# Kernel optimization log

Measured on AMD Instinct MI355X. Metric: run time of the kernel, lower is better.

Reference implementation:

```python
import jax, jax.numpy as jnp
import numpy as np

DIM = 128
N = 4096


def setup_inputs() -> dict:
    key = jax.random.key(0)
    ks = jax.random.split(key, 12)
    d = DIM
    s = 0.02
    inp = jax.random.normal(ks[0], (N, 2 * d), dtype=jnp.float32)
    # H = myLinear: (2d -> 5d -> 1), tanh after each layer
    Hw1 = jax.random.normal(ks[1], (2 * d, 5 * d), dtype=jnp.float32) * s
    Hb1 = jax.random.normal(ks[2], (5 * d,), dtype=jnp.float32) * s
    Hw2 = jax.random.normal(ks[3], (5 * d, 1), dtype=jnp.float32) * s
    Hb2 = jax.random.normal(ks[4], (1,), dtype=jnp.float32) * s
    # augment_f: (d -> 4d -> 8d -> d*d), tanh after each layer
    Aw1 = jax.random.normal(ks[5], (d, 4 * d), dtype=jnp.float32) * s
    Ab1 = jax.random.normal(ks[6], (4 * d,), dtype=jnp.float32) * s
    Aw2 = jax.random.normal(ks[7], (4 * d, 8 * d), dtype=jnp.float32) * s
    Ab2 = jax.random.normal(ks[8], (8 * d,), dtype=jnp.float32) * s
    Aw3 = jax.random.normal(ks[9], (8 * d, d * d), dtype=jnp.float32) * s
    Ab3 = jax.random.normal(ks[10], (d * d,), dtype=jnp.float32) * s
    u = jax.random.uniform(ks[11], (d,), dtype=jnp.float32, minval=-0.001, maxval=0.001)
    return {"t": 0, "inp": inp, "Hw1": Hw1, "Hb1": Hb1, "Hw2": Hw2, "Hb2": Hb2,
            "Aw1": Aw1, "Ab1": Ab1, "Aw2": Aw2, "Ab2": Ab2, "Aw3": Aw3, "Ab3": Ab3, "u": u}


def reference(t, inp, Hw1, Hb1, Hw2, Hb2, Aw1, Ab1, Aw2, Ab2, Aw3, Ab3, u):
    d = DIM
    n = inp.shape[0]

    def H_scalar(z):  # z: [2d] -> scalar
        h = jnp.tanh(z @ Hw1 + Hb1)
        return jnp.tanh(h @ Hw2 + Hb2)[0]

    # per-sample gradient of scalar H w.r.t. input (== batch_jacobian squeeze)
    g = jax.vmap(jax.grad(H_scalar))(inp)  # [N, 2d]
    dx = g[:, :d]
    dv = -g[:, d:]

    x = inp[:, :d]
    h1 = jnp.tanh(x @ Aw1 + Ab1)            # [N, 4d]
    h2 = jnp.tanh(h1 @ Aw2 + Ab2)           # [N, 8d]
    gq = jnp.tanh(h2 @ Aw3 + Ab3).reshape(n, d, d)  # [N, d, d]
    dv = dv + jnp.einsum("nij,j->ni", gq, u)
    return jnp.concatenate([dx, dv], axis=-1)  # [N, 2d]
```

## Files before the change

kernel.cpp:

```cpp
#include <hip/hip_runtime.h>
#include <hip/hip_bf16.h>
#include <cstdint>


typedef __bf16 bf16_t;
typedef __bf16 bf16x4_t __attribute__((ext_vector_type(4)));
typedef __bf16 bf16x8_t __attribute__((ext_vector_type(8)));
typedef float f32x4_t __attribute__((ext_vector_type(4)));
typedef float f32x16_t __attribute__((ext_vector_type(16)));
typedef int intx4_t __attribute__((ext_vector_type(4)));
typedef int intx8_t __attribute__((ext_vector_type(8)));

#define DIMD 128
#define NROW 4096
#define SMEM_G64 24576
#define SMEM3_BYTES 98304

__device__ __forceinline__ float fast_tanh(float x) {
  float t = __builtin_amdgcn_exp2f(x * 2.8853900817779268f);
  return 1.f - 2.f * __builtin_amdgcn_rcpf(t + 1.f);
}

__device__ __forceinline__ uint8_t to_fp8(float x) {
  return (uint8_t)(__builtin_amdgcn_cvt_pk_fp8_f32(x, x, 0, false) & 0xff);
}

__device__ __forceinline__ uint32_t pk4_fp8(float a, float b, float c,
                                            float d) {
  uint32_t lo = (uint32_t)__builtin_amdgcn_cvt_pk_fp8_f32(a, b, 0, false);
  return (uint32_t)__builtin_amdgcn_cvt_pk_fp8_f32(c, d, lo, true);
}

__device__ __forceinline__ void g2l16(const void* gp, void* lp) {
  __builtin_amdgcn_global_load_lds(
      reinterpret_cast<__attribute__((address_space(1))) void*>(
          reinterpret_cast<uintptr_t>(gp)),
      reinterpret_cast<__attribute__((address_space(3))) void*>(
          reinterpret_cast<uintptr_t>(lp)),
      16, 0, 0);
}

template <int CTRL>
__device__ __forceinline__ float dpp_addf(float v) {
  return v + __int_as_float(__builtin_amdgcn_update_dpp(
                 0, __float_as_int(v), CTRL, 0xf, 0xf, true));
}
__device__ __forceinline__ float dpp_sum32(float v) {
  v = dpp_addf<0x111>(v);
  v = dpp_addf<0x112>(v);
  v = dpp_addf<0x114>(v);
  v = dpp_addf<0x118>(v);
  v = dpp_addf<0x142>(v);
  return v;
}

template <int EPI>
__device__ __forceinline__ void gemm64_body(char* smem, int bx, int by,
                                            const bf16_t* A, int lda,
                                            const bf16_t* B, int ldb, int K,
                                            const float* bias, void* outp,
                                            int ldo) {
  constexpr int BK = 32;
  bf16_t* As = (bf16_t*)smem;
  bf16_t* Bs = As + 3 * 2048;
  const int NT = K / BK;

  const int m0 = bx * 64;
  const int n0 = by * 64;
  const int tid = threadIdx.x;
  const int wave = tid >> 6;
  const int lane = tid & 63;
  const int wm = wave >> 1;
  const int wn = wave & 1;

  const int sr = lane >> 2;
  const int sk = (((lane & 3) ^ ((sr >> 1) & 3)) * 8);
  const int fr = lane & 15;
  const int fk = (((lane >> 4) ^ ((fr >> 1) & 3)) * 8);
  const int rb = wave * 16;

  const bf16_t* Ag = A + (size_t)(m0 + rb + sr) * lda + sk;
  const bf16_t* Bg = B + (size_t)(n0 + rb + sr) * ldb + sk;

#define G64_STAGE(buf, k0)                              \
  do {                                                  \
    g2l16(Ag + (k0), As + (buf) * 2048 + rb * BK);      \
    g2l16(Bg + (k0), Bs + (buf) * 2048 + rb * BK);      \
  } while (0)

  f32x4_t acc[2][2] = {};

  G64_STAGE(0, 0);
  G64_STAGE(1, BK);
  asm volatile("s_waitcnt vmcnt(2)" ::: "memory");
  __builtin_amdgcn_s_barrier();
  asm volatile("" ::: "memory");

  for (int t = 0; t < NT; ++t) {
    if (t + 2 < NT) G64_STAGE((t + 2) % 3, (t + 2) * BK);
    const bf16_t* Ab = As + (t % 3) * 2048;
    const bf16_t* Bb = Bs + (t % 3) * 2048;

    bf16x8_t af[2], bb[2];
#pragma unroll
    for (int u = 0; u < 2; ++u) {
      af[u] = *(const bf16x8_t*)(Ab + (wm * 32 + u * 16 + fr) * BK + fk);
      bb[u] = *(const bf16x8_t*)(Bb + (wn * 32 + u * 16 + fr) * BK + fk);
    }
#pragma unroll
    for (int i = 0; i < 2; ++i)
#pragma unroll
      for (int j = 0; j < 2; ++j)
        acc[i][j] = __builtin_amdgcn_mfma_f32_16x16x32_bf16(af[i], bb[j],
                                                            acc[i][j], 0, 0, 0);
    if (t < NT - 1) {
      if (t + 2 < NT)
        asm volatile("s_waitcnt vmcnt(2)" ::: "memory");
      else
        asm volatile("s_waitcnt vmcnt(0)" ::: "memory");
      __builtin_amdgcn_s_barrier();
      asm volatile("" ::: "memory");
    }
  }
#undef G64_STAGE

#pragma unroll
  for (int i = 0; i < 2; ++i) {
    const int row = m0 + wm * 32 + i * 16 + (lane >> 4) * 4;
#pragma unroll
    for (int j = 0; j < 2; ++j) {
      const int col = n0 + wn * 32 + j * 16 + fr;
      if constexpr (EPI == 0) {
        bf16_t* O = (bf16_t*)outp;
        const float b = bias[col];
#pragma unroll
        for (int r = 0; r < 4; ++r)
          O[(size_t)(row + r) * ldo + col] = (bf16_t)fast_tanh(acc[i][j][r] + b);
      } else {
        uint8_t* O = (uint8_t*)outp;
        const float b = bias[col];
#pragma unroll
        for (int r = 0; r < 4; ++r)
          O[(size_t)(row + r) * ldo + col] =
              to_fp8(64.f * fast_tanh(acc[i][j][r] + b));
      }
    }
  }
}

__device__ __forceinline__ void hbwd64_body(char* smem, int bx, int by,
                                            const bf16_t* A, int lda,
                                            const bf16_t* B, int ldb, int K,
                                            float* out, int ldo) {
  constexpr int BK = 32;
  bf16_t* As = (bf16_t*)smem;
  bf16_t* Bs = As + 3 * 2048;
  const int NT = K / BK;

  const int m0 = bx * 64;
  const int n0 = by * 64;
  const int tid = threadIdx.x;
  const int wave = tid >> 6;
  const int lane = tid & 63;
  const int wm = wave >> 2;
  const int wn = wave & 3;

  const int sr = lane >> 2;
  const int sk = (((lane & 3) ^ ((sr >> 1) & 3)) * 8);
  const int fr = lane & 15;
  const int fk = (((lane >> 4) ^ ((fr >> 1) & 3)) * 8);

  const int rbs = (wave & 3) * 16;
  const bf16_t* Sg = (wave < 4) ? A + (size_t)(m0 + rbs + sr) * lda + sk
                                : B + (size_t)(n0 + rbs + sr) * ldb + sk;
  bf16_t* Sl = ((wave < 4) ? As : Bs) + rbs * BK;

  f32x4_t acc[2] = {};

  g2l16(Sg, Sl);
  g2l16(Sg + BK, Sl + 2048);
  asm volatile("s_waitcnt vmcnt(1)" ::: "memory");
  __builtin_amdgcn_s_barrier();
  asm volatile("" ::: "memory");

  for (int t = 0; t < NT; ++t) {
    if (t + 2 < NT) g2l16(Sg + (t + 2) * BK, Sl + ((t + 2) % 3) * 2048);
    const bf16_t* Ab = As + (t % 3) * 2048;
    const bf16_t* Bb = Bs + (t % 3) * 2048;

    const bf16x8_t bb = *(const bf16x8_t*)(Bb + (wn * 16 + fr) * BK + fk);
#pragma unroll
    for (int u = 0; u < 2; ++u) {
      const bf16x8_t af =
          *(const bf16x8_t*)(Ab + (wm * 32 + u * 16 + fr) * BK + fk);
      acc[u] = __builtin_amdgcn_mfma_f32_16x16x32_bf16(af, bb, acc[u], 0, 0, 0);
    }
    if (t < NT - 1) {
      if (t + 2 < NT)
        asm volatile("s_waitcnt vmcnt(1)" ::: "memory");
      else
        asm volatile("s_waitcnt vmcnt(0)" ::: "memory");
      __builtin_amdgcn_s_barrier();
      asm volatile("" ::: "memory");
    }
  }

  const bool dx = (n0 < DIMD);
  const int col = n0 + wn * 16 + fr;
#pragma unroll
  for (int t = 0; t < 2; ++t) {
    const int row = m0 + wm * 32 + t * 16 + (lane >> 4) * 4;
#pragma unroll
    for (int r = 0; r < 4; ++r) {
      const size_t idx = (size_t)(row + r) * ldo + col;
      if (dx) out[idx] = acc[t][r];
      else atomicAdd(&out[idx], -acc[t][r]);
    }
  }
}

__device__ __forceinline__ void a3_body(char* smem, int bx, int by,
                                        const uint8_t* A, const uint8_t* B,
                                        float* out, const float* ab3,
                                        const float* uvec) {
  constexpr int BK = 64, K = 1024, NT = K / BK;
  uint8_t* As = (uint8_t*)smem;
  uint8_t* Bs = As + 49152;

  const int m0 = bx * 256;
  const int n0 = by * 256;
  const int tid = threadIdx.x;
  const int wave = tid >> 6;
  const int lane = tid & 63;
  const int wm = wave >> 1;
  const int wn = wave & 1;

  const int sr = lane >> 2;
  const int sk = ((lane & 3) ^ ((sr >> 1) & 3)) * 16;

  const int rl = lane & 31;
  const int w = (rl >> 1) & 3;
  const int c0 = lane >> 5;
  const int sLo = ((2 * c0) ^ w) * 16;
  const int sHi = ((2 * c0 + 1) ^ w) * 16;

  f32x16_t acc[2][4] = {};

#define A3_STAGE(buf, k0)                                                     \
  do {                                                                        \
    uint8_t* Ad = As + (buf) * 16384;                                         \
    uint8_t* Bd = Bs + (buf) * 16384;                                         \
    _Pragma("unroll") for (int t_ = 0; t_ < 2; ++t_) {                        \
      const int rb_ = wave * 32 + t_ * 16;                                    \
      g2l16(A + (size_t)(m0 + rb_ + sr) * K + ((k0) + sk), Ad + rb_ * BK);    \
      g2l16(B + (size_t)(n0 + rb_ + sr) * K + ((k0) + sk), Bd + rb_ * BK);    \
    }                                                                         \
  } while (0)

  A3_STAGE(0, 0);
  A3_STAGE(1, BK);
  asm volatile("s_waitcnt vmcnt(4)" ::: "memory");
  __builtin_amdgcn_s_barrier();
  asm volatile("" ::: "memory");

  int cur = 0, pre = 2;
#pragma unroll 1
  for (int t = 0; t < NT; ++t) {
    if (t + 2 < NT) A3_STAGE(pre, (t + 2) * BK);
    const uint8_t* Ab = As + cur * 16384;
    const uint8_t* Bb = Bs + cur * 16384;

    __builtin_amdgcn_s_setprio(1);
    intx8_t bfr[4];
#pragma unroll
    for (int j = 0; j < 4; ++j) {
      const int rb2 = (wn * 128 + j * 32 + rl) * BK;
      intx4_t lob = *(const intx4_t*)(Bb + rb2 + sLo);
      intx4_t hib = *(const intx4_t*)(Bb + rb2 + sHi);
      bfr[j] = __builtin_shufflevector(lob, hib, 0, 1, 2, 3, 4, 5, 6, 7);
    }
#pragma unroll
    for (int i = 0; i < 2; ++i) {
      const int ra = (wm * 64 + i * 32 + rl) * BK;
      intx4_t lo = *(const intx4_t*)(Ab + ra + sLo);
      intx4_t hi = *(const intx4_t*)(Ab + ra + sHi);
      intx8_t af = __builtin_shufflevector(lo, hi, 0, 1, 2, 3, 4, 5, 6, 7);
#pragma unroll
      for (int j = 0; j < 4; ++j)
        acc[i][j] = __builtin_amdgcn_mfma_scale_f32_32x32x64_f8f6f4(
            af, bfr[j], acc[i][j], 0, 0, 0, 0x79797979, 0, 0x79797979);
    }
    __builtin_amdgcn_s_setprio(0);

    if (t < NT - 1) {
      if (t + 2 < NT)
        asm volatile("s_waitcnt vmcnt(4)" ::: "memory");
      else
        asm volatile("s_waitcnt vmcnt(0)" ::: "memory");
      __builtin_amdgcn_s_barrier();
      asm volatile("" ::: "memory");
    }
    cur = (cur == 2) ? 0 : cur + 1;
    pre = (pre == 2) ? 0 : pre + 1;
  }
#undef A3_STAGE

  const int q = lane >> 5;
  float uu[4], b3[4];
#pragma unroll
  for (int j = 0; j < 4; ++j) {
    uu[j] = uvec[j * 32 + rl];
    b3[j] = ab3[n0 + wn * 128 + j * 32 + rl];
  }
  const int ocol = 128 + 2 * by + wn;
#pragma unroll
  for (int i = 0; i < 2; ++i) {
    float s16[16];
#pragma unroll
    for (int r = 0; r < 16; ++r) {
      float s = 0.f;
#pragma unroll
      for (int j = 0; j < 4; ++j) s += fast_tanh(acc[i][j][r] + b3[j]) * uu[j];
      s16[r] = s;
    }
#pragma unroll
    for (int r = 0; r < 16; ++r) s16[r] = dpp_sum32(s16[r]);
    if (rl == 31) {
      const int rowb = m0 + wm * 64 + i * 32 + 4 * q;
#pragma unroll
      for (int r = 0; r < 16; ++r)
        atomicAdd(&out[(size_t)(rowb + (r & 3) + 8 * (r >> 2)) * 256 + ocol],
                  s16[r]);
    }
  }
}

__device__ __forceinline__ void tcvt_body(char* smem, const float* in,
                                          bf16_t* out, int R, int C, int bx,
                                          int by) {
  float(*t)[33] = (float(*)[33])smem;
  const int c0 = bx * 32;
  const int r0 = by * 32;
  const int tx = threadIdx.x & 31;
  const int ty = threadIdx.x >> 5;
#pragma unroll
  for (int k = 0; k < 4; ++k)
    t[ty + k * 8][tx] = in[(size_t)(r0 + ty + k * 8) * C + c0 + tx];
  __syncthreads();
#pragma unroll
  for (int k = 0; k < 4; ++k)
    out[(size_t)(c0 + ty + k * 8) * R + r0 + tx] = (bf16_t)t[tx][ty + k * 8];
}

__device__ __forceinline__ void aw3t_body(char* smem, const float* Aw3,
                                          uint8_t* Aw3T8, int b) {
  uint32_t(*T)[33] = (uint32_t(*)[33])smem;
  const int ct = b & 127;
  const int rt = b >> 7;
  const size_t c0 = (size_t)ct * 128;
  const int r0 = rt * 128;
  const int tx = threadIdx.x & 31;
  const int g = threadIdx.x >> 5;
#pragma unroll
  for (int k = 0; k < 4; ++k) {
    const int rr = r0 + 4 * g + 32 * k;
    const float4 v0 = *(const float4*)(Aw3 + (size_t)(rr + 0) * 16384 + c0 + 4 * tx);
    const float4 v1 = *(const float4*)(Aw3 + (size_t)(rr + 1) * 16384 + c0 + 4 * tx);
    const float4 v2 = *(const float4*)(Aw3 + (size_t)(rr + 2) * 16384 + c0 + 4 * tx);
    const float4 v3 = *(const float4*)(Aw3 + (size_t)(rr + 3) * 16384 + c0 + 4 * tx);
    const int r4 = g + 8 * k;
    T[4 * tx + 0][r4] = pk4_fp8(64.f * v0.x, 64.f * v1.x, 64.f * v2.x, 64.f * v3.x);
    T[4 * tx + 1][r4] = pk4_fp8(64.f * v0.y, 64.f * v1.y, 64.f * v2.y, 64.f * v3.y);
    T[4 * tx + 2][r4] = pk4_fp8(64.f * v0.z, 64.f * v1.z, 64.f * v2.z, 64.f * v3.z);
    T[4 * tx + 3][r4] = pk4_fp8(64.f * v0.w, 64.f * v1.w, 64.f * v2.w, 64.f * v3.w);
  }
  __syncthreads();
#pragma unroll
  for (int k2 = 0; k2 < 16; ++k2) {
    const int cc = g + 8 * k2;
    *(uint32_t*)(Aw3T8 + (c0 + cc) * 1024 + r0 + 4 * tx) = T[cc][tx];
  }
}

__device__ __forceinline__ void hgrad_row(int row, const bf16_t* h,
                                          const float* Hw2, const float* Hb2,
                                          bf16_t* wout) {
  const int lane = threadIdx.x & 63;
  float hv[10], wv[10];
  float pre2 = 0.f;
#pragma unroll
  for (int t = 0; t < 10; ++t) {
    const int j = lane + t * 64;
    hv[t] = (float)h[(size_t)row * 640 + j];
    wv[t] = Hw2[j];
    pre2 += hv[t] * wv[t];
  }
#pragma unroll
  for (int d = 1; d < 64; d <<= 1) pre2 += __shfl_xor(pre2, d, 64);
  const float y = fast_tanh(pre2 + Hb2[0]);
  const float s = 1.f - y * y;
#pragma unroll
  for (int t = 0; t < 10; ++t) {
    const int j = lane + t * 64;
    wout[(size_t)row * 640 + j] = (bf16_t)(s * wv[t] * (1.f - hv[t] * hv[t]));
  }
}

__global__ __launch_bounds__(256) void launch0(
    const float* __restrict__ inp, bf16_t* __restrict__ inp_bf,
    const float* __restrict__ Hw1, bf16_t* __restrict__ Hw1T,
    bf16_t* __restrict__ Hw1_bf, const float* __restrict__ Aw1,
    bf16_t* __restrict__ Aw1T, const float* __restrict__ Aw2,
    bf16_t* __restrict__ Aw2T, float* __restrict__ out) {
  __shared__ __align__(16) char smem[4224];
  int b = blockIdx.x;
  if (b < 1024) {
    const int i = b * 256 + threadIdx.x;
    const float4 v = ((const float4*)inp)[i];
    bf16x4_t o = {(bf16_t)v.x, (bf16_t)v.y, (bf16_t)v.z, (bf16_t)v.w};
    ((bf16x4_t*)inp_bf)[i] = o;
  } else if (b < 1184) {
    int s = b - 1024;
    tcvt_body(smem, Hw1, Hw1T, 256, 640, s % 20, s / 20);
  } else if (b < 1248) {
    int s = b - 1184;
    tcvt_body(smem, Aw1, Aw1T, 128, 512, s % 16, s / 16);
  } else if (b < 1760) {
    int s = b - 1248;
    tcvt_body(smem, Aw2, Aw2T, 512, 1024, s % 32, s / 32);
  } else if (b < 1920) {
    const int i = (b - 1760) * 256 + threadIdx.x;
    const float4 v = ((const float4*)Hw1)[i];
    bf16x4_t o = {(bf16_t)v.x, (bf16_t)v.y, (bf16_t)v.z, (bf16_t)v.w};
    ((bf16x4_t*)Hw1_bf)[i] = o;
  } else {
    const int i = (b - 1920) * 256 + threadIdx.x;
    ((float4*)out)[i] = make_float4(0.f, 0.f, 0.f, 0.f);
  }
}

__global__ __launch_bounds__(256) void launch1(
    const bf16_t* __restrict__ inp_bf, const bf16_t* __restrict__ Hw1T,
    const float* __restrict__ Hb1, bf16_t* __restrict__ h_bf,
    const bf16_t* __restrict__ Aw1T, const float* __restrict__ Ab1,
    bf16_t* __restrict__ h1_bf, const float* __restrict__ Aw3,
    uint8_t* __restrict__ Aw3T8) {
  __shared__ __align__(16) char smem[SMEM_G64];
  const int b = blockIdx.x;
  if (b < 640) {
    gemm64_body<0>(smem, b % 64, b / 64, inp_bf, 256, Hw1T, 256, 256, Hb1,
                   h_bf, 640);
  } else if (b < 1152) {
    const int i = b - 640;
    gemm64_body<0>(smem, i % 64, i / 64, inp_bf, 256, Aw1T, 128, 128, Ab1,
                   h1_bf, 512);
  } else {
    aw3t_body(smem, Aw3, Aw3T8, b - 1152);
  }
}

__global__ __launch_bounds__(256) void launch2(
    const bf16_t* __restrict__ h1_bf, const bf16_t* __restrict__ Aw2T,
    const float* __restrict__ Ab2, uint8_t* __restrict__ h2_f8,
    const bf16_t* __restrict__ h_bf, const float* __restrict__ Hw2,
    const float* __restrict__ Hb2, bf16_t* __restrict__ w_bf,
    const float* __restrict__ Aw3, uint8_t* __restrict__ Aw3T8) {
  __shared__ __align__(16) char smem[SMEM_G64];
  const int b = blockIdx.x;
  if (b < 1024) {
    gemm64_body<3>(smem, b % 64, b / 64, h1_bf, 512, Aw2T, 512, 512, Ab2,
                   h2_f8, 1024);
  } else if (b < 2048) {
    const int row = (b - 1024) * 4 + (threadIdx.x >> 6);
    hgrad_row(row, h_bf, Hw2, Hb2, w_bf);
  } else {
    aw3t_body(smem, Aw3, Aw3T8, 512 + (b - 2048));
  }
}

__global__ __launch_bounds__(512, 2) void launch3(
    const bf16_t* __restrict__ w_bf, const bf16_t* __restrict__ Hw1_bf,
    float* __restrict__ out, const uint8_t* __restrict__ h2_f8,
    const uint8_t* __restrict__ Aw3T8, const float* __restrict__ Ab3,
    const float* __restrict__ uvec) {
  __shared__ __align__(16) char smem[SMEM3_BYTES];
  const int b = blockIdx.x;
  if (b < 256) {
    hbwd64_body(smem, b % 64, b / 64, w_bf, 640, Hw1_bf, 640, 640, out, 256);
  } else {
    const int p = b - 256;
    const int by = (p & 7) * 8 + ((p >> 3) & 7);
    const int bx = p >> 6;
    a3_body(smem, bx, by, h2_f8, Aw3T8, out, Ab3, uvec);
  }
}

extern "C" void kernel_launch(void* const* d_in, const int* in_sizes, int n_in,
                              void* d_out, int out_size, void* d_ws,
                              size_t ws_size, hipStream_t stream) {
  (void)in_sizes; (void)n_in; (void)out_size; (void)ws_size;
  const float* inp = (const float*)d_in[1];
  const float* Hw1 = (const float*)d_in[2];
  const float* Hb1 = (const float*)d_in[3];
  const float* Hw2 = (const float*)d_in[4];
  const float* Hb2 = (const float*)d_in[5];
  const float* Aw1 = (const float*)d_in[6];
  const float* Ab1 = (const float*)d_in[7];
  const float* Aw2 = (const float*)d_in[8];
  const float* Ab2 = (const float*)d_in[9];
  const float* Aw3 = (const float*)d_in[10];
  const float* Ab3 = (const float*)d_in[11];
  const float* u = (const float*)d_in[12];
  float* out = (float*)d_out;

  char* ws = (char*)d_ws;
  bf16_t* inp_bf = (bf16_t*)ws;   ws += (size_t)NROW * 256 * 2;
  bf16_t* Hw1_bf = (bf16_t*)ws;   ws += (size_t)256 * 640 * 2;
  bf16_t* Hw1T = (bf16_t*)ws;     ws += (size_t)640 * 256 * 2;
  bf16_t* Aw1T = (bf16_t*)ws;     ws += (size_t)512 * 128 * 2;
  bf16_t* Aw2T = (bf16_t*)ws;     ws += (size_t)1024 * 512 * 2;
  uint8_t* Aw3T8 = (uint8_t*)ws;  ws += (size_t)16384 * 1024;
  bf16_t* h_bf = (bf16_t*)ws;     ws += (size_t)NROW * 640 * 2;
  bf16_t* w_bf = (bf16_t*)ws;     ws += (size_t)NROW * 640 * 2;
  bf16_t* h1_bf = (bf16_t*)ws;    ws += (size_t)NROW * 512 * 2;
  uint8_t* h2_f8 = (uint8_t*)ws;  ws += (size_t)NROW * 1024;

  launch0<<<2944, 256, 0, stream>>>(inp, inp_bf, Hw1, Hw1T, Hw1_bf, Aw1, Aw1T,
                                    Aw2, Aw2T, out);
  launch1<<<1664, 256, 0, stream>>>(inp_bf, Hw1T, Hb1, h_bf, Aw1T, Ab1, h1_bf,
                                    Aw3, Aw3T8);
  launch2<<<2560, 256, 0, stream>>>(h1_bf, Aw2T, Ab2, h2_f8, h_bf, Hw2, Hb2,
                                    w_bf, Aw3, Aw3T8);
  launch3<<<1280, 512, 0, stream>>>(w_bf, Hw1_bf, out, h2_f8, Aw3T8, Ab3, u);
}
```

Measured before the change: 229.7 us.

## Pre-swizzle fp8 operands into MFMA fragment layout and load directly to registers

The fp8 activations h2 and the transposed Aw3 weights are now written in a blocked layout that matches the 32x32x64 MFMA fragment order. The big GEMM can then load each lane's 32 bytes straight from global memory into registers with a double-buffered register pipeline. This drops LDS staging, barriers and swizzle arithmetic, and cuts the shared memory for launch3 from 96KB to 24KB. In exchange it relies on L2/global bandwidth with uncoalesced-looking per-lane 32B reads, uses more registers, and makes the producer stores scattered. The diff calls gemm64_body<4> while the visible epilogue only tests EPI==0; the new blocked fp8 store sits in the else branch, so EPI=4 takes it.

```diff
diff --git a/kernel.cpp b/kernel.cpp
--- a/kernel.cpp
+++ b/kernel.cpp
@@ -14,7 +14,7 @@
 #define DIMD 128
 #define NROW 4096
 #define SMEM_G64 24576
-#define SMEM3_BYTES 98304
+#define SMEM3_BYTES 24576
 
 __device__ __forceinline__ float fast_tanh(float x) {
   float t = __builtin_amdgcn_exp2f(x * 2.8853900817779268f);
@@ -139,10 +139,16 @@
       } else {
         uint8_t* O = (uint8_t*)outp;
         const float b = bias[col];
-#pragma unroll
-        for (int r = 0; r < 4; ++r)
-          O[(size_t)(row + r) * ldo + col] =
+        const int kb = col >> 6;
+        const int khalf = (col >> 5) & 1;
+        const int kin = col & 31;
+#pragma unroll
+        for (int r = 0; r < 4; ++r) {
+          const int rw = row + r;
+          O[(size_t)((rw >> 5) * 16 + kb) * 2048 +
+            (khalf * 32 + (rw & 31)) * 32 + kin] =
               to_fp8(64.f * fast_tanh(acc[i][j][r] + b));
+        }
       }
     }
   }
@@ -219,91 +225,58 @@
   }
 }
 
-__device__ __forceinline__ void a3_body(char* smem, int bx, int by,
-                                        const uint8_t* A, const uint8_t* B,
-                                        float* out, const float* ab3,
-                                        const float* uvec) {
-  constexpr int BK = 64, K = 1024, NT = K / BK;
-  uint8_t* As = (uint8_t*)smem;
-  uint8_t* Bs = As + 49152;
-
-  const int m0 = bx * 256;
-  const int n0 = by * 256;
+__device__ __forceinline__ void a3_body(int bx, int by, const uint8_t* AF,
+                                        const uint8_t* BF, float* out,
+                                        const float* ab3, const float* uvec) {
+  constexpr int NT = 16;
   const int tid = threadIdx.x;
   const int wave = tid >> 6;
   const int lane = tid & 63;
   const int wm = wave >> 1;
   const int wn = wave & 1;
-
-  const int sr = lane >> 2;
-  const int sk = ((lane & 3) ^ ((sr >> 1) & 3)) * 16;
-
   const int rl = lane & 31;
-  const int w = (rl >> 1) & 3;
-  const int c0 = lane >> 5;
-  const int sLo = ((2 * c0) ^ w) * 16;
-  const int sHi = ((2 * c0 + 1) ^ w) * 16;
+  const int m0 = bx * 256;
+  const int n0 = by * 256;
+
+  const uint8_t* bp[6];
+#pragma unroll
+  for (int i = 0; i < 2; ++i)
+    bp[i] = AF + (size_t)(bx * 8 + wm * 2 + i) * 16 * 2048 + lane * 32;
+#pragma unroll
+  for (int j = 0; j < 4; ++j)
+    bp[2 + j] = BF + (size_t)(by * 8 + wn * 4 + j) * 16 * 2048 + lane * 32;
 
   f32x16_t acc[2][4] = {};
-
-#define A3_STAGE(buf, k0)                                                     \
-  do {                                                                        \
-    uint8_t* Ad = As + (buf) * 16384;                                         \
-    uint8_t* Bd = Bs + (buf) * 16384;                                         \
-    _Pragma("unroll") for (int t_ = 0; t_ < 2; ++t_) {                        \
-      const int rb_ = wave * 32 + t_ * 16;                                    \
-      g2l16(A + (size_t)(m0 + rb_ + sr) * K + ((k0) + sk), Ad + rb_ * BK);    \
-      g2l16(B + (size_t)(n0 + rb_ + sr) * K + ((k0) + sk), Bd + rb_ * BK);    \
+  intx4_t cur[12], nxt[12];
+
+#define A3_LOADSET(dst, off)                                   \
+  _Pragma("unroll") for (int q = 0; q < 6; ++q) {              \
+    dst[2 * q] = *(const intx4_t*)(bp[q] + (off));             \
+    dst[2 * q + 1] = *(const intx4_t*)(bp[q] + (off) + 16);    \
+  }
+
+#define A3_MFMASET(S)                                                         \
+  _Pragma("unroll") for (int i = 0; i < 2; ++i) {                             \
+    intx8_t af = __builtin_shufflevector(S[2 * i], S[2 * i + 1], 0, 1, 2, 3,  \
+                                         4, 5, 6, 7);                         \
+    _Pragma("unroll") for (int j = 0; j < 4; ++j) {                           \
+      intx8_t bf = __builtin_shufflevector(S[4 + 2 * j], S[5 + 2 * j], 0, 1,  \
+                                           2, 3, 4, 5, 6, 7);                 \
+      acc[i][j] = __builtin_amdgcn_mfma_scale_f32_32x32x64_f8f6f4(            \
+          af, bf, acc[i][j], 0, 0, 0, 0x79797979, 0, 0x79797979);             \
     }                                                                         \
-  } while (0)
-
-  A3_STAGE(0, 0);
-  A3_STAGE(1, BK);
-  asm volatile("s_waitcnt vmcnt(4)" ::: "memory");
-  __builtin_amdgcn_s_barrier();
-  asm volatile("" ::: "memory");
-
-  int cur = 0, pre = 2;
+  }
+
+  A3_LOADSET(cur, 0);
 #pragma unroll 1
-  for (int t = 0; t < NT; ++t) {
-    if (t + 2 < NT) A3_STAGE(pre, (t + 2) * BK);
-    const uint8_t* Ab = As + cur * 16384;
-    const uint8_t* Bb = Bs + cur * 16384;
-
-    __builtin_amdgcn_s_setprio(1);
-    intx8_t bfr[4];
-#pragma unroll
-    for (int j = 0; j < 4; ++j) {
-      const int rb2 = (wn * 128 + j * 32 + rl) * BK;
-      intx4_t lob = *(const intx4_t*)(Bb + rb2 + sLo);
-      intx4_t hib = *(const intx4_t*)(Bb + rb2 + sHi);
-      bfr[j] = __builtin_shufflevector(lob, hib, 0, 1, 2, 3, 4, 5, 6, 7);
-    }
-#pragma unroll
-    for (int i = 0; i < 2; ++i) {
-      const int ra = (wm * 64 + i * 32 + rl) * BK;
-      intx4_t lo = *(const intx4_t*)(Ab + ra + sLo);
-      intx4_t hi = *(const intx4_t*)(Ab + ra + sHi);
-      intx8_t af = __builtin_shufflevector(lo, hi, 0, 1, 2, 3, 4, 5, 6, 7);
-#pragma unroll
-      for (int j = 0; j < 4; ++j)
-        acc[i][j] = __builtin_amdgcn_mfma_scale_f32_32x32x64_f8f6f4(
-            af, bfr[j], acc[i][j], 0, 0, 0, 0x79797979, 0, 0x79797979);
-    }
-    __builtin_amdgcn_s_setprio(0);
-
-    if (t < NT - 1) {
-      if (t + 2 < NT)
-        asm volatile("s_waitcnt vmcnt(4)" ::: "memory");
-      else
-        asm volatile("s_waitcnt vmcnt(0)" ::: "memory");
-      __builtin_amdgcn_s_barrier();
-      asm volatile("" ::: "memory");
-    }
-    cur = (cur == 2) ? 0 : cur + 1;
-    pre = (pre == 2) ? 0 : pre + 1;
-  }
-#undef A3_STAGE
+  for (int t = 0; t < NT; t += 2) {
+    A3_LOADSET(nxt, (size_t)(t + 1) * 2048);
+    A3_MFMASET(cur);
+    if (t + 2 < NT) A3_LOADSET(cur, (size_t)(t + 2) * 2048);
+    A3_MFMASET(nxt);
+  }
+#undef A3_LOADSET
+#undef A3_MFMASET
 
   const int q = lane >> 5;
   float uu[4], b3[4];
@@ -353,7 +326,7 @@
 }
 
 __device__ __forceinline__ void aw3t_body(char* smem, const float* Aw3,
-                                          uint8_t* Aw3T8, int b) {
+                                          uint8_t* Aw3T8F, int b) {
   uint32_t(*T)[33] = (uint32_t(*)[33])smem;
   const int ct = b & 127;
   const int rt = b >> 7;
@@ -375,10 +348,16 @@
     T[4 * tx + 3][r4] = pk4_fp8(64.f * v0.w, 64.f * v1.w, 64.f * v2.w, 64.f * v3.w);
   }
   __syncthreads();
+  const int kb = (rt << 1) + (tx >> 4);
+  const int khalf = (tx >> 3) & 1;
+  const int kin = (tx & 7) << 2;
 #pragma unroll
   for (int k2 = 0; k2 < 16; ++k2) {
     const int cc = g + 8 * k2;
-    *(uint32_t*)(Aw3T8 + (c0 + cc) * 1024 + r0 + 4 * tx) = T[cc][tx];
+    const int cb = (ct << 2) + (cc >> 5);
+    const int cin = cc & 31;
+    *(uint32_t*)(Aw3T8F + (size_t)(cb * 16 + kb) * 2048 +
+                 (khalf * 32 + cin) * 32 + kin) = T[cc][tx];
   }
 }
 
@@ -444,7 +423,7 @@
     const float* __restrict__ Hb1, bf16_t* __restrict__ h_bf,
     const bf16_t* __restrict__ Aw1T, const float* __restrict__ Ab1,
     bf16_t* __restrict__ h1_bf, const float* __restrict__ Aw3,
-    uint8_t* __restrict__ Aw3T8) {
+    uint8_t* __restrict__ Aw3T8F) {
   __shared__ __align__(16) char smem[SMEM_G64];
   const int b = blockIdx.x;
   if (b < 640) {
@@ -455,33 +434,33 @@
     gemm64_body<0>(smem, i % 64, i / 64, inp_bf, 256, Aw1T, 128, 128, Ab1,
                    h1_bf, 512);
   } else {
-    aw3t_body(smem, Aw3, Aw3T8, b - 1152);
+    aw3t_body(smem, Aw3, Aw3T8F, b - 1152);
   }
 }
 
 __global__ __launch_bounds__(256) void launch2(
     const bf16_t* __restrict__ h1_bf, const bf16_t* __restrict__ Aw2T,
-    const float* __restrict__ Ab2, uint8_t* __restrict__ h2_f8,
+    const float* __restrict__ Ab2, uint8_t* __restrict__ h2F,
     const bf16_t* __restrict__ h_bf, const float* __restrict__ Hw2,
     const float* __restrict__ Hb2, bf16_t* __restrict__ w_bf,
-    const float* __restrict__ Aw3, uint8_t* __restrict__ Aw3T8) {
+    const float* __restrict__ Aw3, uint8_t* __restrict__ Aw3T8F) {
   __shared__ __align__(16) char smem[SMEM_G64];
   const int b = blockIdx.x;
   if (b < 1024) {
-    gemm64_body<3>(smem, b % 64, b / 64, h1_bf, 512, Aw2T, 512, 512, Ab2,
-                   h2_f8, 1024);
+    gemm64_body<4>(smem, b % 64, b / 64, h1_bf, 512, Aw2T, 512, 512, Ab2,
+                   h2F, 0);
   } else if (b < 2048) {
     const int row = (b - 1024) * 4 + (threadIdx.x >> 6);
     hgrad_row(row, h_bf, Hw2, Hb2, w_bf);
   } else {
-    aw3t_body(smem, Aw3, Aw3T8, 512 + (b - 2048));
+    aw3t_body(smem, Aw3, Aw3T8F, 512 + (b - 2048));
   }
 }
 
 __global__ __launch_bounds__(512, 2) void launch3(
     const bf16_t* __restrict__ w_bf, const bf16_t* __restrict__ Hw1_bf,
-    float* __restrict__ out, const uint8_t* __restrict__ h2_f8,
-    const uint8_t* __restrict__ Aw3T8, const float* __restrict__ Ab3,
+    float* __restrict__ out, const uint8_t* __restrict__ h2F,
+    const uint8_t* __restrict__ Aw3T8F, const float* __restrict__ Ab3,
     const float* __restrict__ uvec) {
   __shared__ __align__(16) char smem[SMEM3_BYTES];
   const int b = blockIdx.x;
@@ -491,7 +470,7 @@
     const int p = b - 256;
     const int by = (p & 7) * 8 + ((p >> 3) & 7);
     const int bx = p >> 6;
-    a3_body(smem, bx, by, h2_f8, Aw3T8, out, Ab3, uvec);
+    a3_body(bx, by, h2F, Aw3T8F, out, Ab3, uvec);
   }
 }
 
@@ -514,22 +493,22 @@
   float* out = (float*)d_out;
 
   char* ws = (char*)d_ws;
-  bf16_t* inp_bf = (bf16_t*)ws;   ws += (size_t)NROW * 256 * 2;
-  bf16_t* Hw1_bf = (bf16_t*)ws;   ws += (size_t)256 * 640 * 2;
-  bf16_t* Hw1T = (bf16_t*)ws;     ws += (size_t)640 * 256 * 2;
-  bf16_t* Aw1T = (bf16_t*)ws;     ws += (size_t)512 * 128 * 2;
-  bf16_t* Aw2T = (bf16_t*)ws;     ws += (size_t)1024 * 512 * 2;
-  uint8_t* Aw3T8 = (uint8_t*)ws;  ws += (size_t)16384 * 1024;
-  bf16_t* h_bf = (bf16_t*)ws;     ws += (size_t)NROW * 640 * 2;
-  bf16_t* w_bf = (bf16_t*)ws;     ws += (size_t)NROW * 640 * 2;
-  bf16_t* h1_bf = (bf16_t*)ws;    ws += (size_t)NROW * 512 * 2;
-  uint8_t* h2_f8 = (uint8_t*)ws;  ws += (size_t)NROW * 1024;
+  bf16_t* inp_bf = (bf16_t*)ws;    ws += (size_t)NROW * 256 * 2;
+  bf16_t* Hw1_bf = (bf16_t*)ws;    ws += (size_t)256 * 640 * 2;
+  bf16_t* Hw1T = (bf16_t*)ws;      ws += (size_t)640 * 256 * 2;
+  bf16_t* Aw1T = (bf16_t*)ws;      ws += (size_t)512 * 128 * 2;
+  bf16_t* Aw2T = (bf16_t*)ws;      ws += (size_t)1024 * 512 * 2;
+  uint8_t* Aw3T8F = (uint8_t*)ws;  ws += (size_t)16384 * 1024;
+  bf16_t* h_bf = (bf16_t*)ws;      ws += (size_t)NROW * 640 * 2;
+  bf16_t* w_bf = (bf16_t*)ws;      ws += (size_t)NROW * 640 * 2;
+  bf16_t* h1_bf = (bf16_t*)ws;     ws += (size_t)NROW * 512 * 2;
+  uint8_t* h2F = (uint8_t*)ws;     ws += (size_t)NROW * 1024;
 
   launch0<<<2944, 256, 0, stream>>>(inp, inp_bf, Hw1, Hw1T, Hw1_bf, Aw1, Aw1T,
                                     Aw2, Aw2T, out);
   launch1<<<1664, 256, 0, stream>>>(inp_bf, Hw1T, Hb1, h_bf, Aw1T, Ab1, h1_bf,
-                                    Aw3, Aw3T8);
-  launch2<<<2560, 256, 0, stream>>>(h1_bf, Aw2T, Ab2, h2_f8, h_bf, Hw2, Hb2,
-                                    w_bf, Aw3, Aw3T8);
-  launch3<<<1280, 512, 0, stream>>>(w_bf, Hw1_bf, out, h2_f8, Aw3T8, Ab3, u);
-}
+                                    Aw3, Aw3T8F);
+  launch2<<<2560, 256, 0, stream>>>(h1_bf, Aw2T, Ab2, h2F, h_bf, Hw2, Hb2,
+                                    w_bf, Aw3, Aw3T8F);
+  launch3<<<1280, 512, 0, stream>>>(w_bf, Hw1_bf, out, h2F, Aw3T8F, Ab3, u);
+}
```

Result: slower. 367.5 us (+60.0%).
